# Optimization experiments

Measured on AMD Instinct MI355X. Metric: run time of the kernel, lower is better.

Reference implementation:

```python
import jax, jax.numpy as jnp
import numpy as np

NX, NY = 4096, 4096
T = 1.0
TIME_STEPS = 400
DT = T / TIME_STEPS
DX = 1.0 / (NX - 1)
DY = 1.0 / (NY - 1)
Z = 1.0
FROG = 2
BC = jnp.array([-1.0, 1.0], dtype=jnp.float32)


def _conv_ax0(A, f):
    # valid cross-correlation along axis 0 (matches F.conv1d after transpose)
    L = f.shape[0]
    n = A.shape[0] - L + 1
    out = f[0] * A[0:n, :]
    for k in range(1, L):
        out = out + f[k] * A[k:k + n, :]
    return out


def _conv_ax1(A, f):
    L = f.shape[0]
    n = A.shape[1] - L + 1
    out = f[0] * A[:, 0:n]
    for k in range(1, L):
        out = out + f[k] * A[:, k:k + n]
    return out


def _amper(E, Hx, Hy, f, s):
    # S1: d/dx of Hy ; S2: d/dy of Hx
    S1 = (Z * DT / DX) * _conv_ax0(Hy, f)[0:-1, s:NY - s]
    S2 = (Z * DT / DY) * _conv_ax1(Hx, f)[s:NX - s, 0:-1]
    return E[s:NX - s, s:NY - s] + S1 - S2


def _faraday(E, Hx, Hy, f, s):
    S3 = (DT / (Z * DY)) * _conv_ax1(E, f)[s:NX - s, :]
    S4 = (DT / (Z * DX)) * _conv_ax0(E, f)[:, s:NY - s]
    Ax = Hx[s:NX - s, s - 1:NY - s] - S3
    Ay = Hy[s - 1:NX - s, s:NY - s] + S4
    return Ax, Ay


def setup_inputs() -> dict:
    key = jax.random.key(0)
    k1, k2, k3 = jax.random.split(key, 3)
    X1 = jax.random.normal(k1, (NX, NY), dtype=jnp.float32)
    X2 = jax.random.normal(k2, (NX, NY), dtype=jnp.float32)
    X3 = jax.random.normal(k3, (NX, NY), dtype=jnp.float32)
    w1 = jnp.ones((1,), dtype=jnp.float32)
    return {"X1": X1, "X2": X2, "X3": X3, "w1": w1}


def reference(X1, X2, X3, w1):
    f4 = jnp.concatenate([(w1 - 1.0) / 3.0, -w1, w1, (1.0 - w1) / 3.0])
    E, Hx, Hy = X1, X2, X3
    # boundary-order then interior (frog) Ampere update of E
    E = E.at[1:NX - 1, 1:NY - 1].set(_amper(X1, X2, X3, BC, 1))
    E = E.at[FROG:NX - FROG, FROG:NY - FROG].set(_amper(E, X2, X3, f4, FROG))
    # Faraday updates of Hx, Hy from the ORIGINAL fields (bc order)
    Ax1, Ay1 = _faraday(X1, X2, X3, BC, 1)
    Hx = Hx.at[1:NX - 1, 0:NY - 1].set(Ax1)
    Hy = Hy.at[0:NX - 1, 1:NY - 1].set(Ay1)
    # interior Faraday updates using updated E, Hx, Hy
    Ax2, Ay2 = _faraday(E, Hx, Hy, f4, FROG)
    Hx = Hx.at[FROG:NX - FROG, FROG - 1:NY - FROG].set(Ax2)
    Hy = Hy.at[FROG - 1:NX - FROG, FROG:NY - FROG].set(Ay2)
    return (E, Hx, Hy)
```

## Files before the change

### kernel.cpp

```cpp
#include <hip/hip_runtime.h>

#define NXg 4096
#define NYg 4096
#define BROWS 8
#define ROW0 8
#define NBANDS 510
#define NPANEL 16
#define CCOLS 256
#define LCOLS 264
#define R3 14
#define R2 11
#define R1 11

static constexpr float C = 10.2375f;

struct F7  { float v[7];  };
struct F10 { float v[10]; };

__device__ __forceinline__ F7 mk7(const float4& a, const float4& b, const float4& c) {
    F7 r;
    r.v[0] = a.w; r.v[1] = b.x; r.v[2] = b.y; r.v[3] = b.z;
    r.v[4] = b.w; r.v[5] = c.x; r.v[6] = c.y;
    return r;
}
__device__ __forceinline__ F10 mk10(const float4& a, const float4& b, const float4& c) {
    F10 r;
    r.v[0] = a.y; r.v[1] = a.z; r.v[2] = a.w;
    r.v[3] = b.x; r.v[4] = b.y; r.v[5] = b.z; r.v[6] = b.w;
    r.v[7] = c.x; r.v[8] = c.y; r.v[9] = c.z;
    return r;
}
__device__ __forceinline__ F7 l7(const float* Lrow, int lc) {
    const float4 a = *(const float4*)(Lrow + lc - 4);
    const float4 b = *(const float4*)(Lrow + lc);
    const float4 c = *(const float4*)(Lrow + lc + 4);
    return mk7(a, b, c);
}
__device__ __forceinline__ F10 l10(const float* Lrow, int lc) {
    const float4 a = *(const float4*)(Lrow + lc - 4);
    const float4 b = *(const float4*)(Lrow + lc);
    const float4 c = *(const float4*)(Lrow + lc + 4);
    return mk10(a, b, c);
}

__device__ __forceinline__ void gload_lds16(const float* g, float* l) {
    __builtin_amdgcn_global_load_lds(
        (const __attribute__((address_space(1))) void*)g,
        (__attribute__((address_space(3))) void*)l, 16, 0, 0);
}

__global__ __launch_bounds__(128, 2) void band_kernel(
    const float* __restrict__ X1, const float* __restrict__ X2,
    const float* __restrict__ X3, const float* __restrict__ w1,
    float* __restrict__ E, float* __restrict__ Hx, float* __restrict__ Hy)
{
    __shared__ float L3[R3][LCOLS];
    __shared__ float L2[R2][LCOLS];
    __shared__ float L1[R1][LCOLS];

    const int i0   = ROW0 + blockIdx.y * BROWS;
    const int col0 = blockIdx.x * CCOLS;
    const int wid  = threadIdx.x >> 6;
    const int lane = threadIdx.x & 63;

    for (int q = wid; q < 2 * (R3 + R2 + R1); q += 2) {
        const int part = q & 1;
        const int rid  = q >> 1;
        const float* src;
        float* lrow;
        int grow;
        if (rid < R3)           { src = X3; lrow = &L3[rid][0];           grow = i0 - 3 + rid; }
        else if (rid < R3 + R2) { src = X2; lrow = &L2[rid - R3][0];      grow = i0 - 1 + (rid - R3); }
        else                    { src = X1; lrow = &L1[rid - R3 - R2][0]; grow = i0 - 1 + (rid - R3 - R2); }
        const float* g = src + (size_t)grow * NYg + (col0 - 4 + part * 8) + lane * 4;
        gload_lds16(g, lrow + part * 8);
    }
    __syncthreads();

    const int cq = threadIdx.x & 63;
    const int g  = threadIdx.x >> 6;
    const int lc = 4 + 4 * cq;
    const int rb = 4 * g;
    const int b3 = rb + 3;
    const int b2 = rb + 1;

    const bool gL = (blockIdx.x == 0) && (cq == 0);
    const bool gR = (blockIdx.x == NPANEL - 1) && (cq == 63);

    const float wv = w1[0];
    const float f0 = (wv - 1.0f) / 3.0f;
    const float f1 = -wv;
    const float f2 = wv;
    const float f3 = (1.0f - wv) / 3.0f;

    auto eRow = [&](const F7& x3m2, const F7& x3m1, const F7& x3p0, const F7& x3p1,
                    const F10& x2r, const F7& x1r) -> F7 {
        F7 e;
        #pragma unroll
        for (int m = 0; m < 7; ++m) {
            const float e1 = x1r.v[m] + C * (x3p0.v[m] - x3m1.v[m])
                                      - C * (x2r.v[m + 2] - x2r.v[m + 1]);
            e.v[m] = e1
                + C * (f0 * x3m2.v[m] + f1 * x3m1.v[m] + f2 * x3p0.v[m] + f3 * x3p1.v[m])
                - C * (f0 * x2r.v[m] + f1 * x2r.v[m + 1] + f2 * x2r.v[m + 2] + f3 * x2r.v[m + 3]);
        }
        if (gL) {
            e.v[1] = x1r.v[1];
            e.v[2] = x1r.v[2] + C * (x3p0.v[2] - x3m1.v[2])
                              - C * (x2r.v[4] - x2r.v[3]);
        }
        if (gR) {
            e.v[4] = x1r.v[4];
            e.v[3] = x1r.v[3] + C * (x3p0.v[3] - x3m1.v[3])
                              - C * (x2r.v[5] - x2r.v[4]);
        }
        return e;
    };

    F7 p3a = l7(&L3[b3 - 3][0], lc);
    F7 p3b = l7(&L3[b3 - 2][0], lc);
    F7 p3c = l7(&L3[b3 - 1][0], lc);
    F7 w3[4];
    w3[0] = l7(&L3[b3][0],     lc);
    w3[1] = l7(&L3[b3 + 1][0], lc);
    w3[2] = l7(&L3[b3 + 2][0], lc);
    w3[3] = l7(&L3[b3 + 3][0], lc);

    F10 q2a = l10(&L2[b2 - 1][0], lc);
    F10 q2b = l10(&L2[b2][0],     lc);
    F10 q2c = l10(&L2[b2 + 1][0], lc);
    F10 w2r = l10(&L2[b2 + 2][0], lc);

    F7 q1a = l7(&L1[b2 - 1][0], lc);
    F7 w1r[3];
    w1r[0] = l7(&L1[b2][0],     lc);
    w1r[1] = l7(&L1[b2 + 1][0], lc);
    w1r[2] = l7(&L1[b2 + 2][0], lc);

    F7 ew[4];
    ew[0] = eRow(p3a, p3b, p3c, w3[0], q2a, q1a);
    ew[1] = eRow(p3b, p3c, w3[0], w3[1], q2b, w1r[0]);
    ew[2] = eRow(p3c, w3[0], w3[1], w3[2], q2c, w1r[1]);

    float x2c0[4] = {q2b.v[3], q2b.v[4], q2b.v[5], q2b.v[6]};
    float x2c1[4] = {q2c.v[3], q2c.v[4], q2c.v[5], q2c.v[6]};

    #pragma unroll
    for (int s = 0; s < 4; ++s) {
        const int i = i0 + rb + s;

        ew[3] = eRow(w3[0], w3[1], w3[2], w3[3], w2r, w1r[2]);

        float hx[4], hy[4];
        #pragma unroll
        for (int q = 0; q < 4; ++q) {
            hx[q] = x2c0[q] - C * (w1r[0].v[q + 2] - w1r[0].v[q + 1])
                  - C * (f0 * ew[1].v[q]     + f1 * ew[1].v[q + 1]
                       + f2 * ew[1].v[q + 2] + f3 * ew[1].v[q + 3]);
            hy[q] = w3[0].v[q + 1] + C * (w1r[1].v[q + 1] - w1r[0].v[q + 1])
                  + C * (f0 * ew[0].v[q + 1] + f1 * ew[1].v[q + 1]
                       + f2 * ew[2].v[q + 1] + f3 * ew[3].v[q + 1]);
        }
        if (gL) {
            hx[0] = x2c0[0] - C * (w1r[0].v[2] - w1r[0].v[1]);
            hy[0] = w3[0].v[1];
            hy[1] = w3[0].v[2] + C * (w1r[1].v[2] - w1r[0].v[2]);
        }
        if (gR) {
            hx[3] = x2c0[3];
            hy[3] = w3[0].v[4];
            hx[2] = x2c0[2] - C * (w1r[0].v[4] - w1r[0].v[3]);
            hy[2] = w3[0].v[3] + C * (w1r[1].v[3] - w1r[0].v[3]);
        }

        const size_t idx = (size_t)i * NYg + col0 + 4 * cq;
        *(float4*)(E  + idx) = make_float4(ew[1].v[1], ew[1].v[2], ew[1].v[3], ew[1].v[4]);
        *(float4*)(Hx + idx) = make_float4(hx[0], hx[1], hx[2], hx[3]);
        *(float4*)(Hy + idx) = make_float4(hy[0], hy[1], hy[2], hy[3]);

        ew[0] = ew[1]; ew[1] = ew[2]; ew[2] = ew[3];
        w3[0] = w3[1]; w3[1] = w3[2]; w3[2] = w3[3];
        w1r[0] = w1r[1]; w1r[1] = w1r[2];
        #pragma unroll
        for (int q = 0; q < 4; ++q) { x2c0[q] = x2c1[q]; x2c1[q] = w2r.v[3 + q]; }
        if (s < 3) {
            w3[3]  = l7 (&L3[b3 + 4 + s][0], lc);
            w2r    = l10(&L2[b2 + 3 + s][0], lc);
            w1r[2] = l7 (&L1[b2 + 3 + s][0], lc);
        }
    }
}

#define TRE 8
#define EROWSE 12
#define ECOLSE 136

__global__ __launch_bounds__(256) void edge_kernel(
    const float* __restrict__ X1, const float* __restrict__ X2,
    const float* __restrict__ X3, const float* __restrict__ w1,
    float* __restrict__ E, float* __restrict__ Hx, float* __restrict__ Hy)
{
    __shared__ float elds[EROWSE][ECOLSE];
    const int t    = threadIdx.x;
    const int row0 = blockIdx.y ? (NXg - TRE) : 0;
    const int col0 = blockIdx.x * 128;

    const float wv = w1[0];
    const float f0 = (wv - 1.0f) / 3.0f;
    const float f1 = -wv;
    const float f2 = wv;
    const float f3 = (1.0f - wv) / 3.0f;

    for (int cidx = t; cidx < EROWSE * ECOLSE; cidx += 256) {
        const int r  = cidx / ECOLSE;
        const int cc = cidx - r * ECOLSE;
        const int gr = row0 - 2 + r;
        const int gc = col0 - 4 + cc;
        float e = 0.0f;
        if (gr >= 0 && gr < NXg && gc >= 0 && gc < NYg) {
            const size_t idx = (size_t)gr * NYg + gc;
            const float x1 = X1[idx];
            if (gr == 0 || gr == NXg - 1 || gc == 0 || gc == NYg - 1) {
                e = x1;
            } else {
                float e1 = x1 + C * (X3[idx] - X3[idx - NYg])
                              - C * (X2[idx] - X2[idx - 1]);
                if (gr >= 2 && gr <= NXg - 3 && gc >= 2 && gc <= NYg - 3) {
                    e1 += C * (f0 * X3[idx - 2 * NYg] + f1 * X3[idx - NYg]
                             + f2 * X3[idx] + f3 * X3[idx + NYg])
                        - C * (f0 * X2[idx - 2] + f1 * X2[idx - 1]
                             + f2 * X2[idx] + f3 * X2[idx + 1]);
                }
                e = e1;
            }
        }
        elds[r][cc] = e;
    }
    __syncthreads();

    for (int cidx = t; cidx < TRE * 128; cidx += 256) {
        const int hr  = cidx >> 7;
        const int tc  = cidx & 127;
        const int gr  = row0 + hr;
        const int gcc = col0 + tc;
        const size_t idx = (size_t)gr * NYg + gcc;
        const int lr  = hr + 2;
        const int lc2 = tc + 4;

        const float ec = elds[lr][lc2];
        E[idx] = ec;

        const float x1 = X1[idx];

        float hx = X2[idx];
        if (gr >= 1 && gr <= NXg - 2 && gcc <= NYg - 2)
            hx -= C * (X1[idx + 1] - x1);
        if (gr >= 2 && gr <= NXg - 3 && gcc >= 1 && gcc <= NYg - 3) {
            hx -= C * (f0 * elds[lr][lc2 - 1] + f1 * ec
                     + f2 * elds[lr][lc2 + 1] + f3 * elds[lr][lc2 + 2]);
        }
        Hx[idx] = hx;

        float hy = X3[idx];
        if (gr <= NXg - 2 && gcc >= 1 && gcc <= NYg - 2)
            hy += C * (X1[idx + NYg] - x1);
        if (gr >= 1 && gr <= NXg - 3 && gcc >= 2 && gcc <= NYg - 3) {
            hy += C * (f0 * elds[lr - 1][lc2] + f1 * ec
                     + f2 * elds[lr + 1][lc2] + f3 * elds[lr + 2][lc2]);
        }
        Hy[idx] = hy;
    }
}

extern "C" void kernel_launch(void* const* d_in, const int* in_sizes, int n_in,
                              void* d_out, int out_size, void* d_ws, size_t ws_size,
                              hipStream_t stream) {
    const float* X1 = (const float*)d_in[0];
    const float* X2 = (const float*)d_in[1];
    const float* X3 = (const float*)d_in[2];
    const float* w1 = (const float*)d_in[3];

    float* E  = (float*)d_out;
    float* Hx = (float*)d_out + (size_t)NXg * NYg;
    float* Hy = (float*)d_out + 2 * (size_t)NXg * NYg;

    edge_kernel<<<dim3(32, 2), 256, 0, stream>>>(X1, X2, X3, w1, E, Hx, Hy);
    band_kernel<<<dim3(NPANEL, NBANDS), 128, 0, stream>>>(X1, X2, X3, w1, E, Hx, Hy);
}
```

Baseline: 98.04 us.

## Make band kernel loop over bands with double-buffered async LDS staging

The band kernel changes from one 128-thread block per 8-row band (8160 blocks) to 1024 single-wave blocks. Each block walks about 16 consecutive bands of a 128-column panel. The three input tiles now share one contiguous LDS buffer, and two such buffers are alternated, so the next band's global-to-LDS loads are issued while the current band is computed. Partial vmcnt waits take the place of block barriers. The aim is to hide global load latency and cut per-block launch and staging overhead, at the cost of far fewer resident waves per CU to hide latency, and a wait scheme that relies on loads completing in order.

```diff
diff --git a/kernel.cpp b/kernel.cpp
--- a/kernel.cpp
+++ b/kernel.cpp
@@ -5,12 +5,14 @@
 #define BROWS 8
 #define ROW0 8
 #define NBANDS 510
-#define NPANEL 16
-#define CCOLS 256
-#define LCOLS 264
-#define R3 14
-#define R2 11
-#define R1 11
+#define NPANEL 32
+#define CCOLS 128
+#define LCOLS 136
+#define TROWS 36
+#define NCHUNK (TROWS * LCOLS / 4)
+#define NJ ((NCHUNK + 63) / 64)
+#define VPB 32
+#define BPB ((NBANDS + VPB - 1) / VPB)
 
 static constexpr float C = 10.2375f;
 
@@ -49,49 +51,49 @@
         (__attribute__((address_space(3))) void*)l, 16, 0, 0);
 }
 
-__global__ __launch_bounds__(128, 2) void band_kernel(
+__global__ __launch_bounds__(64) void band_kernel(
     const float* __restrict__ X1, const float* __restrict__ X2,
     const float* __restrict__ X3, const float* __restrict__ w1,
     float* __restrict__ E, float* __restrict__ Hx, float* __restrict__ Hy)
 {
-    __shared__ float L3[R3][LCOLS];
-    __shared__ float L2[R2][LCOLS];
-    __shared__ float L1[R1][LCOLS];
-
-    const int i0   = ROW0 + blockIdx.y * BROWS;
+    __shared__ float Ba[TROWS * LCOLS];
+    __shared__ float Bb[TROWS * LCOLS];
+
+    const int tid  = threadIdx.x;
     const int col0 = blockIdx.x * CCOLS;
-    const int wid  = threadIdx.x >> 6;
-    const int lane = threadIdx.x & 63;
-
-    for (int q = wid; q < 2 * (R3 + R2 + R1); q += 2) {
-        const int part = q & 1;
-        const int rid  = q >> 1;
-        const float* src;
-        float* lrow;
-        int grow;
-        if (rid < R3)           { src = X3; lrow = &L3[rid][0];           grow = i0 - 3 + rid; }
-        else if (rid < R3 + R2) { src = X2; lrow = &L2[rid - R3][0];      grow = i0 - 1 + (rid - R3); }
-        else                    { src = X1; lrow = &L1[rid - R3 - R2][0]; grow = i0 - 1 + (rid - R3 - R2); }
-        const float* g = src + (size_t)grow * NYg + (col0 - 4 + part * 8) + lane * 4;
-        gload_lds16(g, lrow + part * 8);
-    }
-    __syncthreads();
-
-    const int cq = threadIdx.x & 63;
-    const int g  = threadIdx.x >> 6;
-    const int lc = 4 + 4 * cq;
-    const int rb = 4 * g;
-    const int b3 = rb + 3;
-    const int b2 = rb + 1;
-
-    const bool gL = (blockIdx.x == 0) && (cq == 0);
-    const bool gR = (blockIdx.x == NPANEL - 1) && (cq == 63);
+    const int k0   = blockIdx.y * BPB;
+    const int kend = (k0 + BPB < NBANDS) ? (k0 + BPB) : NBANDS;
 
     const float wv = w1[0];
     const float f0 = (wv - 1.0f) / 3.0f;
     const float f1 = -wv;
     const float f2 = wv;
     const float f3 = (1.0f - wv) / 3.0f;
+
+    const int cq = tid & 31;
+    const int g  = tid >> 5;
+    const int lc = 4 + 4 * cq;
+    const int rb = 4 * g;
+    const bool gL = (blockIdx.x == 0) && (cq == 0);
+    const bool gR = (blockIdx.x == NPANEL - 1) && (cq == 31);
+
+    auto stage = [&](float* lbuf, int band) {
+        const int i0 = ROW0 + band * BROWS;
+        #pragma unroll
+        for (int j = 0; j < NJ; ++j) {
+            const int c = j * 64 + tid;
+            if (c < NCHUNK) {
+                const int row = c / (LCOLS / 4);
+                const int cc  = c - row * (LCOLS / 4);
+                const float* base; int grow;
+                if (row < 14)      { base = X3; grow = i0 - 3 + row; }
+                else if (row < 25) { base = X2; grow = i0 - 15 + row; }
+                else               { base = X1; grow = i0 - 26 + row; }
+                const float* gp = base + (size_t)grow * NYg + (col0 - 4) + cc * 4;
+                gload_lds16(gp, lbuf + (size_t)j * 256);
+            }
+        }
+    };
 
     auto eRow = [&](const F7& x3m2, const F7& x3m1, const F7& x3p0, const F7& x3p1,
                     const F10& x2r, const F7& x1r) -> F7 {
@@ -117,77 +119,100 @@
         return e;
     };
 
-    F7 p3a = l7(&L3[b3 - 3][0], lc);
-    F7 p3b = l7(&L3[b3 - 2][0], lc);
-    F7 p3c = l7(&L3[b3 - 1][0], lc);
-    F7 w3[4];
-    w3[0] = l7(&L3[b3][0],     lc);
-    w3[1] = l7(&L3[b3 + 1][0], lc);
-    w3[2] = l7(&L3[b3 + 2][0], lc);
-    w3[3] = l7(&L3[b3 + 3][0], lc);
-
-    F10 q2a = l10(&L2[b2 - 1][0], lc);
-    F10 q2b = l10(&L2[b2][0],     lc);
-    F10 q2c = l10(&L2[b2 + 1][0], lc);
-    F10 w2r = l10(&L2[b2 + 2][0], lc);
-
-    F7 q1a = l7(&L1[b2 - 1][0], lc);
-    F7 w1r[3];
-    w1r[0] = l7(&L1[b2][0],     lc);
-    w1r[1] = l7(&L1[b2 + 1][0], lc);
-    w1r[2] = l7(&L1[b2 + 2][0], lc);
-
-    F7 ew[4];
-    ew[0] = eRow(p3a, p3b, p3c, w3[0], q2a, q1a);
-    ew[1] = eRow(p3b, p3c, w3[0], w3[1], q2b, w1r[0]);
-    ew[2] = eRow(p3c, w3[0], w3[1], w3[2], q2c, w1r[1]);
-
-    float x2c0[4] = {q2b.v[3], q2b.v[4], q2b.v[5], q2b.v[6]};
-    float x2c1[4] = {q2c.v[3], q2c.v[4], q2c.v[5], q2c.v[6]};
-
-    #pragma unroll
-    for (int s = 0; s < 4; ++s) {
-        const int i = i0 + rb + s;
-
-        ew[3] = eRow(w3[0], w3[1], w3[2], w3[3], w2r, w1r[2]);
-
-        float hx[4], hy[4];
+    auto compute = [&](const float* lb, int band) {
+        const int i0 = ROW0 + band * BROWS;
+        const float* T3r = lb;
+        const float* T2r = lb + 14 * LCOLS;
+        const float* T1r = lb + 25 * LCOLS;
+        const int b3 = rb + 3;
+        const int b2 = rb + 1;
+
+        F7 p3a = l7(&T3r[(b3 - 3) * LCOLS], lc);
+        F7 p3b = l7(&T3r[(b3 - 2) * LCOLS], lc);
+        F7 p3c = l7(&T3r[(b3 - 1) * LCOLS], lc);
+        F7 w3[4];
+        w3[0] = l7(&T3r[(b3    ) * LCOLS], lc);
+        w3[1] = l7(&T3r[(b3 + 1) * LCOLS], lc);
+        w3[2] = l7(&T3r[(b3 + 2) * LCOLS], lc);
+        w3[3] = l7(&T3r[(b3 + 3) * LCOLS], lc);
+
+        F10 q2a = l10(&T2r[(b2 - 1) * LCOLS], lc);
+        F10 q2b = l10(&T2r[(b2    ) * LCOLS], lc);
+        F10 q2c = l10(&T2r[(b2 + 1) * LCOLS], lc);
+        F10 w2r = l10(&T2r[(b2 + 2) * LCOLS], lc);
+
+        F7 q1a = l7(&T1r[(b2 - 1) * LCOLS], lc);
+        F7 w1r[3];
+        w1r[0] = l7(&T1r[(b2    ) * LCOLS], lc);
+        w1r[1] = l7(&T1r[(b2 + 1) * LCOLS], lc);
+        w1r[2] = l7(&T1r[(b2 + 2) * LCOLS], lc);
+
+        F7 ew[4];
+        ew[0] = eRow(p3a, p3b, p3c, w3[0], q2a, q1a);
+        ew[1] = eRow(p3b, p3c, w3[0], w3[1], q2b, w1r[0]);
+        ew[2] = eRow(p3c, w3[0], w3[1], w3[2], q2c, w1r[1]);
+
+        float x2c0[4] = {q2b.v[3], q2b.v[4], q2b.v[5], q2b.v[6]};
+        float x2c1[4] = {q2c.v[3], q2c.v[4], q2c.v[5], q2c.v[6]};
+
         #pragma unroll
-        for (int q = 0; q < 4; ++q) {
-            hx[q] = x2c0[q] - C * (w1r[0].v[q + 2] - w1r[0].v[q + 1])
-                  - C * (f0 * ew[1].v[q]     + f1 * ew[1].v[q + 1]
-                       + f2 * ew[1].v[q + 2] + f3 * ew[1].v[q + 3]);
-            hy[q] = w3[0].v[q + 1] + C * (w1r[1].v[q + 1] - w1r[0].v[q + 1])
-                  + C * (f0 * ew[0].v[q + 1] + f1 * ew[1].v[q + 1]
-                       + f2 * ew[2].v[q + 1] + f3 * ew[3].v[q + 1]);
-        }
-        if (gL) {
-            hx[0] = x2c0[0] - C * (w1r[0].v[2] - w1r[0].v[1]);
-            hy[0] = w3[0].v[1];
-            hy[1] = w3[0].v[2] + C * (w1r[1].v[2] - w1r[0].v[2]);
-        }
-        if (gR) {
-            hx[3] = x2c0[3];
-            hy[3] = w3[0].v[4];
-            hx[2] = x2c0[2] - C * (w1r[0].v[4] - w1r[0].v[3]);
-            hy[2] = w3[0].v[3] + C * (w1r[1].v[3] - w1r[0].v[3]);
-        }
-
-        const size_t idx = (size_t)i * NYg + col0 + 4 * cq;
-        *(float4*)(E  + idx) = make_float4(ew[1].v[1], ew[1].v[2], ew[1].v[3], ew[1].v[4]);
-        *(float4*)(Hx + idx) = make_float4(hx[0], hx[1], hx[2], hx[3]);
-        *(float4*)(Hy + idx) = make_float4(hy[0], hy[1], hy[2], hy[3]);
-
-        ew[0] = ew[1]; ew[1] = ew[2]; ew[2] = ew[3];
-        w3[0] = w3[1]; w3[1] = w3[2]; w3[2] = w3[3];
-        w1r[0] = w1r[1]; w1r[1] = w1r[2];
-        #pragma unroll
-        for (int q = 0; q < 4; ++q) { x2c0[q] = x2c1[q]; x2c1[q] = w2r.v[3 + q]; }
-        if (s < 3) {
-            w3[3]  = l7 (&L3[b3 + 4 + s][0], lc);
-            w2r    = l10(&L2[b2 + 3 + s][0], lc);
-            w1r[2] = l7 (&L1[b2 + 3 + s][0], lc);
-        }
+        for (int s = 0; s < 4; ++s) {
+            const int i = i0 + rb + s;
+
+            ew[3] = eRow(w3[0], w3[1], w3[2], w3[3], w2r, w1r[2]);
+
+            float hx[4], hy[4];
+            #pragma unroll
+            for (int q = 0; q < 4; ++q) {
+                hx[q] = x2c0[q] - C * (w1r[0].v[q + 2] - w1r[0].v[q + 1])
+                      - C * (f0 * ew[1].v[q]     + f1 * ew[1].v[q + 1]
+                           + f2 * ew[1].v[q + 2] + f3 * ew[1].v[q + 3]);
+                hy[q] = w3[0].v[q + 1] + C * (w1r[1].v[q + 1] - w1r[0].v[q + 1])
+                      + C * (f0 * ew[0].v[q + 1] + f1 * ew[1].v[q + 1]
+                           + f2 * ew[2].v[q + 1] + f3 * ew[3].v[q + 1]);
+            }
+            if (gL) {
+                hx[0] = x2c0[0] - C * (w1r[0].v[2] - w1r[0].v[1]);
+                hy[0] = w3[0].v[1];
+                hy[1] = w3[0].v[2] + C * (w1r[1].v[2] - w1r[0].v[2]);
+            }
+            if (gR) {
+                hx[3] = x2c0[3];
+                hy[3] = w3[0].v[4];
+                hx[2] = x2c0[2] - C * (w1r[0].v[4] - w1r[0].v[3]);
+                hy[2] = w3[0].v[3] + C * (w1r[1].v[3] - w1r[0].v[3]);
+            }
+
+            const size_t idx = (size_t)i * NYg + col0 + 4 * cq;
+            *(float4*)(E  + idx) = make_float4(ew[1].v[1], ew[1].v[2], ew[1].v[3], ew[1].v[4]);
+            *(float4*)(Hx + idx) = make_float4(hx[0], hx[1], hx[2], hx[3]);
+            *(float4*)(Hy + idx) = make_float4(hy[0], hy[1], hy[2], hy[3]);
+
+            ew[0] = ew[1]; ew[1] = ew[2]; ew[2] = ew[3];
+            w3[0] = w3[1]; w3[1] = w3[2]; w3[2] = w3[3];
+            w1r[0] = w1r[1]; w1r[1] = w1r[2];
+            #pragma unroll
+            for (int q = 0; q < 4; ++q) { x2c0[q] = x2c1[q]; x2c1[q] = w2r.v[3 + q]; }
+            if (s < 3) {
+                w3[3]  = l7 (&T3r[(b3 + 4 + s) * LCOLS], lc);
+                w2r    = l10(&T2r[(b2 + 3 + s) * LCOLS], lc);
+                w1r[2] = l7 (&T1r[(b2 + 3 + s) * LCOLS], lc);
+            }
+        }
+    };
+
+    stage(Ba, k0);
+    for (int k = k0; k < kend; k += 2) {
+        stage(Bb, k + 1);
+        asm volatile("s_waitcnt vmcnt(20)" ::: "memory");
+        compute(Ba, k);
+        if (k + 2 < kend) {
+            stage(Ba, k + 2);
+            asm volatile("s_waitcnt vmcnt(20)" ::: "memory");
+        } else {
+            asm volatile("s_waitcnt vmcnt(0)" ::: "memory");
+        }
+        compute(Bb, k + 1);
     }
 }
 
@@ -285,5 +310,5 @@
     float* Hy = (float*)d_out + 2 * (size_t)NXg * NYg;
 
     edge_kernel<<<dim3(32, 2), 256, 0, stream>>>(X1, X2, X3, w1, E, Hx, Hy);
-    band_kernel<<<dim3(NPANEL, NBANDS), 128, 0, stream>>>(X1, X2, X3, w1, E, Hx, Hy);
-}
+    band_kernel<<<dim3(NPANEL, VPB), 64, 0, stream>>>(X1, X2, X3, w1, E, Hx, Hy);
+}
```

Result: slower. 376.6 us (+284.2%).
